# Performance work log

Hardware: AMD Instinct MI355X
Metric: run time of the kernel (lower is better)

## Reference

```python
import jax, jax.numpy as jnp
import numpy as np

B, T, E, H, V = 32, 128, 512, 1024, 32000


def setup_inputs() -> dict:
    key = jax.random.key(0)
    ks = jax.random.split(key, 14)
    s = 0.02  # param init scale to keep gates in a sane range
    return {
        "features": jax.random.normal(ks[0], (B, E), jnp.float32),
        "captions": jax.random.randint(ks[1], (B, T), 0, V, jnp.int64),
        "embed_table": jax.random.normal(ks[2], (V, E), jnp.float32) * s,
        "pos_enc": jax.random.normal(ks[3], (1, T, E), jnp.float32) * s,
        "W_ih0": jax.random.normal(ks[4], (4 * H, E), jnp.float32) * s,
        "W_hh0": jax.random.normal(ks[5], (4 * H, H), jnp.float32) * s,
        "b_ih0": jax.random.normal(ks[6], (4 * H,), jnp.float32) * s,
        "b_hh0": jax.random.normal(ks[7], (4 * H,), jnp.float32) * s,
        "W_ih1": jax.random.normal(ks[8], (4 * H, H), jnp.float32) * s,
        "W_hh1": jax.random.normal(ks[9], (4 * H, H), jnp.float32) * s,
        "b_ih1": jax.random.normal(ks[10], (4 * H,), jnp.float32) * s,
        "b_hh1": jax.random.normal(ks[11], (4 * H,), jnp.float32) * s,
        "W_out": jax.random.normal(ks[12], (V, H), jnp.float32) * s,
        "b_out": jax.random.normal(ks[13], (V,), jnp.float32) * s,
    }


def _lstm_cell(h, c, x, W_ih, W_hh, b_ih, b_hh):
    # PyTorch gate order: i, f, g, o
    g = x @ W_ih.T + b_ih + h @ W_hh.T + b_hh  # (B, 4H)
    i, f, gg, o = jnp.split(g, 4, axis=-1)
    c_new = jax.nn.sigmoid(f) * c + jax.nn.sigmoid(i) * jnp.tanh(gg)
    h_new = jax.nn.sigmoid(o) * jnp.tanh(c_new)
    return h_new, c_new


def reference(features, captions, embed_table, pos_enc,
              W_ih0, W_hh0, b_ih0, b_hh0,
              W_ih1, W_hh1, b_ih1, b_hh1,
              W_out, b_out):
    # Teacher forcing ratio = 1.0 (the default): the input at step t is
    # captions[:, t-1], so the whole sequence of inputs is known upfront.
    bsz, seqlen = captions.shape
    hdim = W_hh0.shape[1]
    vocab = W_out.shape[0]
    dt = embed_table.dtype

    # Embedding lookup for all steps; only pos_enc[:, :1, :] is ever added.
    x = embed_table[captions[:, : seqlen - 1]] + pos_enc[0, 0]  # (B, T-1, E)
    x = jnp.swapaxes(x, 0, 1)  # (T-1, B, E) time-major for scan

    h0 = jnp.zeros((bsz, hdim), dt)
    c0 = jnp.zeros((bsz, hdim), dt)
    h1 = jnp.zeros((bsz, hdim), dt)
    c1 = jnp.zeros((bsz, hdim), dt)

    def step(carry, x_t):
        h0, c0, h1, c1 = carry
        h0, c0 = _lstm_cell(h0, c0, x_t, W_ih0, W_hh0, b_ih0, b_hh0)
        h1, c1 = _lstm_cell(h1, c1, h0, W_ih1, W_hh1, b_ih1, b_hh1)
        return (h0, c0, h1, c1), h1

    _, hs = jax.lax.scan(step, (h0, c0, h1, c1), x)  # (T-1, B, H)

    # One big GEMM for the decode projection of all steps.
    logits = jnp.einsum('tbh,vh->btv', hs, W_out) + b_out  # (B, T-1, V)
    outputs = jnp.concatenate(
        [jnp.zeros((bsz, 1, vocab), dt), logits], axis=1)  # outputs[:,0,:]=0
    return outputs
```

## Files before the change

### kernel.cpp

```cpp
#include <hip/hip_runtime.h>
#include <hip/hip_bf16.h>
#include <math.h>

typedef __attribute__((ext_vector_type(4))) float f32x4;
typedef __attribute__((ext_vector_type(8))) short s16x8;
typedef __attribute__((ext_vector_type(4))) unsigned short u16x4;

#define MFMA16(a, b, c) __builtin_amdgcn_mfma_f32_16x16x32_bf16(a, b, c, 0, 0, 0)

static constexpr int BB = 32, TT = 128, EE = 512, HH = 1024, VV = 32000;
static constexpr int FH = 4 * HH;
static constexpr int MROWS = (TT - 1) * BB;
static constexpr int MPAD = 4096;
static constexpr int BH = BB * HH;
static constexpr int NBLK = 256;

__device__ __forceinline__ unsigned short f2bf(float f) {
  unsigned int u = __float_as_uint(f);
  u = (u + 0x7FFFu + ((u >> 16) & 1u)) >> 16;
  return (unsigned short)u;
}
__device__ __forceinline__ float sigf(float x) { return 1.f / (1.f + __expf(-x)); }

__device__ __forceinline__ s16x8 pack8f(const float* p) {
  float4 x = *(const float4*)p;
  float4 y = *(const float4*)(p + 4);
  s16x8 r;
  r[0] = (short)f2bf(x.x); r[1] = (short)f2bf(x.y);
  r[2] = (short)f2bf(x.z); r[3] = (short)f2bf(x.w);
  r[4] = (short)f2bf(y.x); r[5] = (short)f2bf(y.y);
  r[6] = (short)f2bf(y.z); r[7] = (short)f2bf(y.w);
  return r;
}

__device__ __forceinline__ void gl_lds16(const void* g, void* l) {
  __builtin_amdgcn_global_load_lds(
      (const __attribute__((address_space(1))) unsigned int*)g,
      (__attribute__((address_space(3))) unsigned int*)l, 16, 0, 0);
}


__global__ void zero_k(uint4* __restrict__ p, int n16) {
  int i = blockIdx.x * blockDim.x + threadIdx.x;
  int stride = gridDim.x * blockDim.x;
  uint4 z = {0u, 0u, 0u, 0u};
  for (; i < n16; i += stride) p[i] = z;
}

__global__ void cvt_bf16_v4(const float4* __restrict__ in, u16x4* __restrict__ out, int n4) {
  int i = blockIdx.x * blockDim.x + threadIdx.x;
  int stride = gridDim.x * blockDim.x;
  for (; i < n4; i += stride) {
    float4 v = in[i];
    u16x4 o;
    o[0] = f2bf(v.x); o[1] = f2bf(v.y); o[2] = f2bf(v.z); o[3] = f2bf(v.w);
    out[i] = o;
  }
}

__global__ __launch_bounds__(256) void embed_k(const int* __restrict__ captions,
                                               const float* __restrict__ etab,
                                               const float* __restrict__ pos,
                                               unsigned short* __restrict__ X) {
  const int m = blockIdx.x;
  const int t = m >> 5, b = m & 31;
  if (t < TT - 1) {
    const int tok = captions[b * TT + t];
    const float* er = etab + (size_t)tok * EE;
    for (int e = threadIdx.x; e < EE; e += 256)
      X[(size_t)m * EE + e] = f2bf(er[e] + pos[e]);
  } else {
    for (int e = threadIdx.x; e < EE; e += 256) X[(size_t)m * EE + e] = 0;
  }
}

__global__ void zero_out_t0(float* __restrict__ out) {
  out[(size_t)blockIdx.y * TT * VV + blockIdx.x * 256 + threadIdx.x] = 0.f;
}


__global__ __launch_bounds__(256) void gemm_bt(const unsigned short* __restrict__ A,
                                               const unsigned short* __restrict__ Bm,
                                               int K, int N,
                                               const float* __restrict__ bias0,
                                               const float* __restrict__ bias1,
                                               float* __restrict__ Cout) {
  __shared__ unsigned short As[128 * 64];
  __shared__ unsigned short Bs[128 * 64];
  const int tid = threadIdx.x;
  const int lane = tid & 63, wave = tid >> 6;
  const int wm = wave & 1, wn = wave >> 1;
  const int m0 = blockIdx.x * 128, n0 = blockIdx.y * 128;
  const int sch = (lane & 7) * 8;
  const int srbase = wave * 32 + (lane >> 3);
  f32x4 acc[4][4] = {};

  for (int k0 = 0; k0 < K; k0 += 64) {
    __syncthreads();
#pragma unroll
    for (int i = 0; i < 4; ++i) {
      const int r = srbase + i * 8;
      gl_lds16(&A[(size_t)(m0 + r) * K + k0 + sch], &As[(wave * 4 + i) * 512]);
      gl_lds16(&Bm[(size_t)(n0 + r) * K + k0 + sch], &Bs[(wave * 4 + i) * 512]);
    }
    __syncthreads();
#pragma unroll
    for (int kk = 0; kk < 64; kk += 32) {
      s16x8 af[4], bf[4];
#pragma unroll
      for (int f = 0; f < 4; ++f) {
        af[f] = *(const s16x8*)(&As[(wm * 64 + f * 16 + (lane & 15)) * 64 + kk + (lane >> 4) * 8]);
        bf[f] = *(const s16x8*)(&Bs[(wn * 64 + f * 16 + (lane & 15)) * 64 + kk + (lane >> 4) * 8]);
      }
#pragma unroll
      for (int mi = 0; mi < 4; ++mi)
#pragma unroll
        for (int ni = 0; ni < 4; ++ni)
          acc[mi][ni] = MFMA16(af[mi], bf[ni], acc[mi][ni]);
    }
  }

#pragma unroll
  for (int mi = 0; mi < 4; ++mi) {
#pragma unroll
    for (int ni = 0; ni < 4; ++ni) {
      const int col = n0 + wn * 64 + ni * 16 + (lane & 15);
      float bs = bias0[col] + bias1[col];
      const int mbase = m0 + wm * 64 + mi * 16 + (lane >> 4) * 4;
#pragma unroll
      for (int r = 0; r < 4; ++r) {
        int m = mbase + r;
        if (m < MROWS) Cout[(size_t)m * N + col] = acc[mi][ni][r] + bs;
      }
    }
  }
}


__global__ __launch_bounds__(256) void proj_gemm(const unsigned short* __restrict__ hsA,
                                                 const unsigned short* __restrict__ Woutb,
                                                 const float* __restrict__ bout,
                                                 float* __restrict__ out) {
  __shared__ unsigned short As[128 * 64];
  __shared__ unsigned short Bs[128 * 64];
  const int tid = threadIdx.x;
  const int lane = tid & 63, wave = tid >> 6;
  const int wm = wave & 1, wn = wave >> 1;
  const int T = blockIdx.x;
  const int ng = T >> 6, r6 = T & 63;
  const int j = r6 >> 1, dn = r6 & 1;
  const int n = ng * 2 + dn;
  const int m0 = j * 128, n0 = n * 128;
  const int sch = (lane & 7) * 8;
  const int srbase = wave * 32 + (lane >> 3);
  f32x4 acc[4][4] = {};

  for (int k0 = 0; k0 < HH; k0 += 64) {
    __syncthreads();
#pragma unroll
    for (int i = 0; i < 4; ++i) {
      const int rr = srbase + i * 8;
      gl_lds16(&hsA[(size_t)(m0 + rr) * HH + k0 + sch], &As[(wave * 4 + i) * 512]);
      gl_lds16(&Woutb[(size_t)(n0 + rr) * HH + k0 + sch], &Bs[(wave * 4 + i) * 512]);
    }
    __syncthreads();
#pragma unroll
    for (int kk = 0; kk < 64; kk += 32) {
      s16x8 af[4], bf[4];
#pragma unroll
      for (int f = 0; f < 4; ++f) {
        af[f] = *(const s16x8*)(&As[(wm * 64 + f * 16 + (lane & 15)) * 64 + kk + (lane >> 4) * 8]);
        bf[f] = *(const s16x8*)(&Bs[(wn * 64 + f * 16 + (lane & 15)) * 64 + kk + (lane >> 4) * 8]);
      }
#pragma unroll
      for (int mi = 0; mi < 4; ++mi)
#pragma unroll
        for (int ni = 0; ni < 4; ++ni)
          acc[mi][ni] = MFMA16(af[mi], bf[ni], acc[mi][ni]);
    }
  }

#pragma unroll
  for (int mi = 0; mi < 4; ++mi) {
#pragma unroll
    for (int ni = 0; ni < 4; ++ni) {
      const int col = n0 + wn * 64 + ni * 16 + (lane & 15);
      const float bs = bout[col];
      const int mbase = m0 + wm * 64 + mi * 16 + (lane >> 4) * 4;
#pragma unroll
      for (int r2 = 0; r2 < 4; ++r2) {
        const int m = mbase + r2;
        if (m < MROWS) {
          const int tt = m >> 5, b2 = m & 31;
          out[((size_t)b2 * TT + tt + 1) * VV + col] = acc[mi][ni][r2] + bs;
        }
      }
    }
  }
}


__global__ __launch_bounds__(256, 1) void lstm_persist(
    const float* __restrict__ Whh0f, const float* __restrict__ Wih1f,
    const float* __restrict__ Whh1f, const float* __restrict__ G0pre,
    const float* __restrict__ bih1, const float* __restrict__ bhh1,
    unsigned short* __restrict__ h0seq, unsigned short* __restrict__ hseq1,
    unsigned short* __restrict__ hs_all,
    unsigned int* __restrict__ flags0, unsigned int* __restrict__ flags1,
    unsigned int* __restrict__ epoch0, unsigned int* __restrict__ epoch1) {
  __shared__ float parts[4][2][2][16][16];
  const int bid = blockIdx.x;
  const int layer = bid >> 7;
  const int blk = bid & 127;
  const int tid = threadIdx.x, lane = tid & 63, wave = tid >> 6;
  const int jb = blk * 8;
  const int colIdx = lane & 15;
  const int kq = lane >> 4;
  const int wrow0 = (colIdx >> 3) * HH + jb + (colIdx & 7);

  const int cb = tid >> 3, cjj = tid & 7;
  float creg = 0.f;
  float bsum[4];
  if (layer == 1) {
#pragma unroll
    for (int gi = 0; gi < 4; ++gi)
      bsum[gi] = bih1[gi * HH + jb + cjj] + bhh1[gi * HH + jb + cjj];
  }

  s16x8 wreg[16][2];
  const int kb = (layer == 0) ? wave * 256 : (wave & 1) * 512;
  if (layer == 0) {
#pragma unroll
    for (int fi = 0; fi < 2; ++fi) {
      const float* wp = Whh0f + (size_t)(wrow0 + fi * 2 * HH) * HH + kb + kq * 8;
#pragma unroll
      for (int ks = 0; ks < 8; ++ks) wreg[ks][fi] = pack8f(wp + ks * 32);
    }
  } else {
    const float* Wsrc = (wave < 2) ? Wih1f : Whh1f;
#pragma unroll
    for (int fi = 0; fi < 2; ++fi) {
      const float* wp = Wsrc + (size_t)(wrow0 + fi * 2 * HH) * HH + kb + kq * 8;
#pragma unroll
      for (int ks = 0; ks < 16; ++ks) wreg[ks][fi] = pack8f(wp + ks * 32);
    }
  }

  const int frag_off = (kb >> 3) * 256 + kq * 256 + (lane & 15) * 8;

  if (layer == 0) {
    volatile unsigned int* ep0 = &epoch0[(bid & 7) * 32];
    for (int t = 0; t < TT - 1; ++t) {
      float gpre[4];
#pragma unroll
      for (int gi = 0; gi < 4; ++gi)
        gpre[gi] = G0pre[((size_t)t * BB + cb) * FH + gi * HH + jb + cjj];

      if (t > 0 && tid == 0) {
        while (*ep0 < (unsigned)t) __builtin_amdgcn_s_sleep(2);
      }
      __syncthreads();
      asm volatile("" ::: "memory");

      const unsigned short* a0 = h0seq + (size_t)t * BH + frag_off;
      const unsigned short* a1 = a0 + 128;
      f32x4 acc00 = {}, acc01 = {}, acc10 = {}, acc11 = {};
#pragma unroll
      for (int ks = 0; ks < 8; ++ks) {
        s16x8 av0 = *(const s16x8*)(a0 + ks * 1024);
        s16x8 av1 = *(const s16x8*)(a1 + ks * 1024);
        acc00 = MFMA16(av0, wreg[ks][0], acc00);
        acc01 = MFMA16(av0, wreg[ks][1], acc01);
        acc10 = MFMA16(av1, wreg[ks][0], acc10);
        acc11 = MFMA16(av1, wreg[ks][1], acc11);
      }
#pragma unroll
      for (int r = 0; r < 4; ++r) {
        parts[wave][0][0][kq * 4 + r][colIdx] = acc00[r];
        parts[wave][0][1][kq * 4 + r][colIdx] = acc01[r];
        parts[wave][1][0][kq * 4 + r][colIdx] = acc10[r];
        parts[wave][1][1][kq * 4 + r][colIdx] = acc11[r];
      }
      __syncthreads();
      float g[4];
#pragma unroll
      for (int gi = 0; gi < 4; ++gi) {
        float s = gpre[gi];
        const int fi = gi >> 1, c = (gi & 1) * 8 + cjj;
#pragma unroll
        for (int w4 = 0; w4 < 4; ++w4) s += parts[w4][cb >> 4][fi][cb & 15][c];
        g[gi] = s;
      }
      const float i_ = sigf(g[0]), f_ = sigf(g[1]), gg = tanhf(g[2]), o_ = sigf(g[3]);
      creg = f_ * creg + i_ * gg;
      *(volatile unsigned short*)&h0seq[(size_t)(t + 1) * BH + blk * 256 + tid] =
          f2bf(o_ * tanhf(creg));

      asm volatile("s_waitcnt vmcnt(0)" ::: "memory");
      __syncthreads();
      if (tid == 0) *(volatile unsigned int*)&flags0[blk * 32] = (unsigned)(t + 1);
      if (bid == 0) {
        if (tid < 64) {
          const unsigned tgt = (unsigned)(t + 1);
          for (;;) {
            unsigned a = __hip_atomic_load(&flags0[(tid * 2 + 0) * 32], __ATOMIC_RELAXED,
                                           __HIP_MEMORY_SCOPE_AGENT);
            unsigned b = __hip_atomic_load(&flags0[(tid * 2 + 1) * 32], __ATOMIC_RELAXED,
                                           __HIP_MEMORY_SCOPE_AGENT);
            if (__all(min(a, b) >= tgt)) break;
            __builtin_amdgcn_s_sleep(1);
          }
          if (tid < 8) *(volatile unsigned int*)&epoch0[tid * 32] = tgt;
        }
        __syncthreads();
      }
    }
  } else {
    volatile unsigned int* ep0 = &epoch0[(bid & 7) * 32];
    volatile unsigned int* ep1 = &epoch1[(bid & 7) * 32];
    for (int t = 1; t < TT; ++t) {
      if (tid == 0) {
        while (*ep0 < (unsigned)t) __builtin_amdgcn_s_sleep(2);
        while (*ep1 < (unsigned)(t - 1)) __builtin_amdgcn_s_sleep(2);
      }
      __syncthreads();
      asm volatile("" ::: "memory");

      const unsigned short* base = (wave < 2)
                                       ? (h0seq + (size_t)t * BH)
                                       : (hseq1 + (size_t)(t - 1) * BH);
      const unsigned short* a0 = base + frag_off;
      const unsigned short* a1 = a0 + 128;
      f32x4 acc00 = {}, acc01 = {}, acc10 = {}, acc11 = {};
#pragma unroll
      for (int ks = 0; ks < 16; ++ks) {
        s16x8 av0 = *(const s16x8*)(a0 + ks * 1024);
        s16x8 av1 = *(const s16x8*)(a1 + ks * 1024);
        acc00 = MFMA16(av0, wreg[ks][0], acc00);
        acc01 = MFMA16(av0, wreg[ks][1], acc01);
        acc10 = MFMA16(av1, wreg[ks][0], acc10);
        acc11 = MFMA16(av1, wreg[ks][1], acc11);
      }
#pragma unroll
      for (int r = 0; r < 4; ++r) {
        parts[wave][0][0][kq * 4 + r][colIdx] = acc00[r];
        parts[wave][0][1][kq * 4 + r][colIdx] = acc01[r];
        parts[wave][1][0][kq * 4 + r][colIdx] = acc10[r];
        parts[wave][1][1][kq * 4 + r][colIdx] = acc11[r];
      }
      __syncthreads();
      float g[4];
#pragma unroll
      for (int gi = 0; gi < 4; ++gi) {
        float s = bsum[gi];
        const int fi = gi >> 1, c = (gi & 1) * 8 + cjj;
#pragma unroll
        for (int w4 = 0; w4 < 4; ++w4) s += parts[w4][cb >> 4][fi][cb & 15][c];
        g[gi] = s;
      }
      const float i_ = sigf(g[0]), f_ = sigf(g[1]), gg = tanhf(g[2]), o_ = sigf(g[3]);
      creg = f_ * creg + i_ * gg;
      const unsigned short hv = f2bf(o_ * tanhf(creg));
      *(volatile unsigned short*)&hseq1[(size_t)t * BH + blk * 256 + tid] = hv;
      hs_all[(size_t)t * BH + (size_t)cb * HH + jb + cjj] = hv;

      asm volatile("s_waitcnt vmcnt(0)" ::: "memory");
      __syncthreads();
      if (tid == 0) *(volatile unsigned int*)&flags1[blk * 32] = (unsigned)t;
      if (bid == 128) {
        if (tid < 64) {
          const unsigned tgt = (unsigned)t;
          for (;;) {
            unsigned a = __hip_atomic_load(&flags1[(tid * 2 + 0) * 32], __ATOMIC_RELAXED,
                                           __HIP_MEMORY_SCOPE_AGENT);
            unsigned b = __hip_atomic_load(&flags1[(tid * 2 + 1) * 32], __ATOMIC_RELAXED,
                                           __HIP_MEMORY_SCOPE_AGENT);
            if (__all(min(a, b) >= tgt)) break;
            __builtin_amdgcn_s_sleep(1);
          }
          if (tid < 8) *(volatile unsigned int*)&epoch1[tid * 32] = tgt;
        }
        __syncthreads();
      }
    }
  }
}


extern "C" void kernel_launch(void* const* d_in, const int* in_sizes, int n_in,
                              void* d_out, int out_size, void* d_ws, size_t ws_size,
                              hipStream_t stream) {
  const int* captions = (const int*)d_in[1];
  const float* etab = (const float*)d_in[2];
  const float* pos = (const float*)d_in[3];
  const float* Wih0 = (const float*)d_in[4];
  const float* Whh0 = (const float*)d_in[5];
  const float* bih0 = (const float*)d_in[6];
  const float* bhh0 = (const float*)d_in[7];
  const float* Wih1 = (const float*)d_in[8];
  const float* Whh1 = (const float*)d_in[9];
  const float* bih1 = (const float*)d_in[10];
  const float* bhh1 = (const float*)d_in[11];
  const float* Wout = (const float*)d_in[12];
  const float* bout = (const float*)d_in[13];
  float* out = (float*)d_out;

  char* w = (char*)d_ws;
  auto alloc = [&](size_t bytes) {
    char* p = w;
    w += (bytes + 255) & ~(size_t)255;
    return p;
  };
  unsigned int* flags0 = (unsigned int*)alloc(128 * 128);
  unsigned int* flags1 = (unsigned int*)alloc(128 * 128);
  unsigned int* epoch0 = (unsigned int*)alloc(1024);
  unsigned int* epoch1 = (unsigned int*)alloc(1024);
  unsigned short* h0seq = (unsigned short*)alloc((size_t)TT * BH * 2);
  unsigned short* hseq1 = (unsigned short*)alloc((size_t)TT * BH * 2);
  unsigned short* hs_all = (unsigned short*)alloc((size_t)4160 * HH * 2);

  unsigned short* Xb = (unsigned short*)alloc((size_t)MPAD * EE * 2);
  unsigned short* Wih0b = (unsigned short*)alloc((size_t)FH * EE * 2);
  unsigned short* Woutb = (unsigned short*)alloc((size_t)VV * HH * 2);
  float* G0pre = (float*)alloc((size_t)MROWS * FH * 4);

  const int span0 = (128 * 128 * 2 + 2048 + BH * 2) / 16;
  hipLaunchKernelGGL(zero_k, dim3(25), dim3(256), 0, stream, (uint4*)flags0, span0);
  hipLaunchKernelGGL(zero_k, dim3(16), dim3(256), 0, stream, (uint4*)hseq1,
                     (int)((BH * 2) / 16));
  hipLaunchKernelGGL(cvt_bf16_v4, dim3(1024), dim3(256), 0, stream, (const float4*)Wih0,
                     (u16x4*)Wih0b, FH * EE / 4);
  hipLaunchKernelGGL(cvt_bf16_v4, dim3(4096), dim3(256), 0, stream, (const float4*)Wout,
                     (u16x4*)Woutb, VV * HH / 4);
  hipLaunchKernelGGL(embed_k, dim3(MPAD), dim3(256), 0, stream, captions, etab, pos, Xb);
  hipLaunchKernelGGL(gemm_bt, dim3(32, 32), dim3(256), 0, stream, Xb, Wih0b, EE, FH, bih0,
                     bhh0, G0pre);
  hipLaunchKernelGGL(lstm_persist, dim3(NBLK), dim3(256), 0, stream, Whh0, Wih1, Whh1, G0pre,
                     bih1, bhh1, h0seq, hseq1, hs_all, flags0, flags1, epoch0, epoch1);
  hipLaunchKernelGGL(proj_gemm, dim3(8000), dim3(256), 0, stream, hs_all + (size_t)BH, Woutb,
                     bout, out);
  hipLaunchKernelGGL(zero_out_t0, dim3(125, 32), dim3(256), 0, stream, out);
}
```

Measured before the change: 1.442 ms.

## Replace epoch-broadcast barrier with direct per-block flag polling in persistent LSTM

The persistent LSTM kernel drops the two-hop barrier, in which one leader block gathered all flags and then published an epoch word. Instead, wave 0 of every block polls all 128 per-block flags directly, which removes one hop of global-memory latency from each timestep's critical path. The price is many more concurrent polling loads on the flag lines. Separately, the zeroing and bf16 conversion launches are merged into single kernels, and the projection GEMM's block-to-tile mapping becomes a plain row-major j/n split.

Measured after the change: 1.367 ms. 5.2% less time.

```diff
diff --git a/kernel.cpp b/kernel.cpp
--- a/kernel.cpp
+++ b/kernel.cpp
@@ -39,22 +39,34 @@
       (__attribute__((address_space(3))) unsigned int*)l, 16, 0, 0);
 }
 
-
-__global__ void zero_k(uint4* __restrict__ p, int n16) {
+__device__ __forceinline__ unsigned ldflag(const unsigned int* p) {
+  return __hip_atomic_load(p, __ATOMIC_RELAXED, __HIP_MEMORY_SCOPE_AGENT);
+}
+
+
+__global__ void zero2_k(uint4* __restrict__ p0, int n0, uint4* __restrict__ p1, int n1) {
   int i = blockIdx.x * blockDim.x + threadIdx.x;
   int stride = gridDim.x * blockDim.x;
   uint4 z = {0u, 0u, 0u, 0u};
-  for (; i < n16; i += stride) p[i] = z;
-}
-
-__global__ void cvt_bf16_v4(const float4* __restrict__ in, u16x4* __restrict__ out, int n4) {
+  for (int k = i; k < n0; k += stride) p0[k] = z;
+  for (int k = i; k < n1; k += stride) p1[k] = z;
+}
+
+__global__ void cvt2_k(const float4* __restrict__ a, u16x4* __restrict__ ao, int na4,
+                       const float4* __restrict__ b, u16x4* __restrict__ bo, int nb4) {
   int i = blockIdx.x * blockDim.x + threadIdx.x;
   int stride = gridDim.x * blockDim.x;
-  for (; i < n4; i += stride) {
-    float4 v = in[i];
+  for (int k = i; k < na4; k += stride) {
+    float4 v = a[k];
     u16x4 o;
     o[0] = f2bf(v.x); o[1] = f2bf(v.y); o[2] = f2bf(v.z); o[3] = f2bf(v.w);
-    out[i] = o;
+    ao[k] = o;
+  }
+  for (int k = i; k < nb4; k += stride) {
+    float4 v = b[k];
+    u16x4 o;
+    o[0] = f2bf(v.x); o[1] = f2bf(v.y); o[2] = f2bf(v.z); o[3] = f2bf(v.w);
+    bo[k] = o;
   }
 }
 
@@ -147,9 +159,7 @@
   const int lane = tid & 63, wave = tid >> 6;
   const int wm = wave & 1, wn = wave >> 1;
   const int T = blockIdx.x;
-  const int ng = T >> 6, r6 = T & 63;
-  const int j = r6 >> 1, dn = r6 & 1;
-  const int n = ng * 2 + dn;
+  const int j = T / 250, n = T % 250;
   const int m0 = j * 128, n0 = n * 128;
   const int sch = (lane & 7) * 8;
   const int srbase = wave * 32 + (lane >> 3);
@@ -206,8 +216,7 @@
     const float* __restrict__ bih1, const float* __restrict__ bhh1,
     unsigned short* __restrict__ h0seq, unsigned short* __restrict__ hseq1,
     unsigned short* __restrict__ hs_all,
-    unsigned int* __restrict__ flags0, unsigned int* __restrict__ flags1,
-    unsigned int* __restrict__ epoch0, unsigned int* __restrict__ epoch1) {
+    unsigned int* __restrict__ flags0, unsigned int* __restrict__ flags1) {
   __shared__ float parts[4][2][2][16][16];
   const int bid = blockIdx.x;
   const int layer = bid >> 7;
@@ -249,15 +258,20 @@
   const int frag_off = (kb >> 3) * 256 + kq * 256 + (lane & 15) * 8;
 
   if (layer == 0) {
-    volatile unsigned int* ep0 = &epoch0[(bid & 7) * 32];
     for (int t = 0; t < TT - 1; ++t) {
       float gpre[4];
 #pragma unroll
       for (int gi = 0; gi < 4; ++gi)
         gpre[gi] = G0pre[((size_t)t * BB + cb) * FH + gi * HH + jb + cjj];
 
-      if (t > 0 && tid == 0) {
-        while (*ep0 < (unsigned)t) __builtin_amdgcn_s_sleep(2);
+      if (t > 0 && wave == 0) {
+        const unsigned tgt = (unsigned)t;
+        for (;;) {
+          unsigned a = ldflag(&flags0[(lane * 2 + 0) * 32]);
+          unsigned b = ldflag(&flags0[(lane * 2 + 1) * 32]);
+          if (__all(min(a, b) >= tgt)) break;
+          __builtin_amdgcn_s_sleep(1);
+        }
       }
       __syncthreads();
       asm volatile("" ::: "memory");
@@ -299,29 +313,20 @@
       asm volatile("s_waitcnt vmcnt(0)" ::: "memory");
       __syncthreads();
       if (tid == 0) *(volatile unsigned int*)&flags0[blk * 32] = (unsigned)(t + 1);
-      if (bid == 0) {
-        if (tid < 64) {
-          const unsigned tgt = (unsigned)(t + 1);
-          for (;;) {
-            unsigned a = __hip_atomic_load(&flags0[(tid * 2 + 0) * 32], __ATOMIC_RELAXED,
-                                           __HIP_MEMORY_SCOPE_AGENT);
-            unsigned b = __hip_atomic_load(&flags0[(tid * 2 + 1) * 32], __ATOMIC_RELAXED,
-                                           __HIP_MEMORY_SCOPE_AGENT);
-            if (__all(min(a, b) >= tgt)) break;
-            __builtin_amdgcn_s_sleep(1);
-          }
-          if (tid < 8) *(volatile unsigned int*)&epoch0[tid * 32] = tgt;
+    }
+  } else {
+    for (int t = 1; t < TT; ++t) {
+      if (wave == 0) {
+        const unsigned t0 = (unsigned)t, t1 = (unsigned)(t - 1);
+        for (;;) {
+          unsigned a0 = ldflag(&flags0[(lane * 2 + 0) * 32]);
+          unsigned b0 = ldflag(&flags0[(lane * 2 + 1) * 32]);
+          unsigned a1 = ldflag(&flags1[(lane * 2 + 0) * 32]);
+          unsigned b1 = ldflag(&flags1[(lane * 2 + 1) * 32]);
+          bool ok = (min(a0, b0) >= t0) && (min(a1, b1) >= t1);
+          if (__all(ok)) break;
+          __builtin_amdgcn_s_sleep(1);
         }
-        __syncthreads();
-      }
-    }
-  } else {
-    volatile unsigned int* ep0 = &epoch0[(bid & 7) * 32];
-    volatile unsigned int* ep1 = &epoch1[(bid & 7) * 32];
-    for (int t = 1; t < TT; ++t) {
-      if (tid == 0) {
-        while (*ep0 < (unsigned)t) __builtin_amdgcn_s_sleep(2);
-        while (*ep1 < (unsigned)(t - 1)) __builtin_amdgcn_s_sleep(2);
       }
       __syncthreads();
       asm volatile("" ::: "memory");
@@ -367,21 +372,6 @@
       asm volatile("s_waitcnt vmcnt(0)" ::: "memory");
       __syncthreads();
       if (tid == 0) *(volatile unsigned int*)&flags1[blk * 32] = (unsigned)t;
-      if (bid == 128) {
-        if (tid < 64) {
-          const unsigned tgt = (unsigned)t;
-          for (;;) {
-            unsigned a = __hip_atomic_load(&flags1[(tid * 2 + 0) * 32], __ATOMIC_RELAXED,
-                                           __HIP_MEMORY_SCOPE_AGENT);
-            unsigned b = __hip_atomic_load(&flags1[(tid * 2 + 1) * 32], __ATOMIC_RELAXED,
-                                           __HIP_MEMORY_SCOPE_AGENT);
-            if (__all(min(a, b) >= tgt)) break;
-            __builtin_amdgcn_s_sleep(1);
-          }
-          if (tid < 8) *(volatile unsigned int*)&epoch1[tid * 32] = tgt;
-        }
-        __syncthreads();
-      }
     }
   }
 }
@@ -413,8 +403,6 @@
   };
   unsigned int* flags0 = (unsigned int*)alloc(128 * 128);
   unsigned int* flags1 = (unsigned int*)alloc(128 * 128);
-  unsigned int* epoch0 = (unsigned int*)alloc(1024);
-  unsigned int* epoch1 = (unsigned int*)alloc(1024);
   unsigned short* h0seq = (unsigned short*)alloc((size_t)TT * BH * 2);
   unsigned short* hseq1 = (unsigned short*)alloc((size_t)TT * BH * 2);
   unsigned short* hs_all = (unsigned short*)alloc((size_t)4160 * HH * 2);
@@ -424,19 +412,17 @@
   unsigned short* Woutb = (unsigned short*)alloc((size_t)VV * HH * 2);
   float* G0pre = (float*)alloc((size_t)MROWS * FH * 4);
 
-  const int span0 = (128 * 128 * 2 + 2048 + BH * 2) / 16;
-  hipLaunchKernelGGL(zero_k, dim3(25), dim3(256), 0, stream, (uint4*)flags0, span0);
-  hipLaunchKernelGGL(zero_k, dim3(16), dim3(256), 0, stream, (uint4*)hseq1,
-                     (int)((BH * 2) / 16));
-  hipLaunchKernelGGL(cvt_bf16_v4, dim3(1024), dim3(256), 0, stream, (const float4*)Wih0,
-                     (u16x4*)Wih0b, FH * EE / 4);
-  hipLaunchKernelGGL(cvt_bf16_v4, dim3(4096), dim3(256), 0, stream, (const float4*)Wout,
-                     (u16x4*)Woutb, VV * HH / 4);
+  hipLaunchKernelGGL(zero2_k, dim3(40), dim3(256), 0, stream,
+                     (uint4*)flags0, (int)((128 * 128 * 2 + BH * 2) / 16),
+                     (uint4*)hseq1, (int)((BH * 2) / 16));
+  hipLaunchKernelGGL(cvt2_k, dim3(4096), dim3(256), 0, stream,
+                     (const float4*)Wih0, (u16x4*)Wih0b, FH * EE / 4,
+                     (const float4*)Wout, (u16x4*)Woutb, VV * HH / 4);
   hipLaunchKernelGGL(embed_k, dim3(MPAD), dim3(256), 0, stream, captions, etab, pos, Xb);
   hipLaunchKernelGGL(gemm_bt, dim3(32, 32), dim3(256), 0, stream, Xb, Wih0b, EE, FH, bih0,
                      bhh0, G0pre);
   hipLaunchKernelGGL(lstm_persist, dim3(NBLK), dim3(256), 0, stream, Whh0, Wih1, Whh1, G0pre,
-                     bih1, bhh1, h0seq, hseq1, hs_all, flags0, flags1, epoch0, epoch1);
+                     bih1, bhh1, h0seq, hseq1, hs_all, flags0, flags1);
   hipLaunchKernelGGL(proj_gemm, dim3(8000), dim3(256), 0, stream, hs_all + (size_t)BH, Woutb,
                      bout, out);
   hipLaunchKernelGGL(zero_out_t0, dim3(125, 32), dim3(256), 0, stream, out);
```
